# Kernel optimization log

Measured on AMD Instinct MI355X. Metric: run time of the kernel, lower is better.

The kernel has to match this reference:

```python
import jax, jax.numpy as jnp
import numpy as np

D = 1024          # d_model
EXPAND = 2
DI = EXPAND * D   # d_inner = 2048
K = 4             # d_conv
B, L = 4, 2048
EPS = 1e-6


def setup_inputs() -> dict:
    key = jax.random.key(0)
    ks = jax.random.split(key, 16)
    n = lambda i, shape, scale=0.02: (jax.random.normal(ks[i], shape, jnp.float32) * scale)
    return {
        "x": jax.random.normal(ks[0], (B, L, D), jnp.float32),
        "norm_w": jnp.ones((D,), jnp.float32),
        "up_w": n(1, (D, DI)), "up_b": jnp.zeros((DI,), jnp.float32),
        "gate_w": n(2, (D, DI)), "gate_b": jnp.zeros((DI,), jnp.float32),
        "down_w": n(3, (DI, D)), "down_b": jnp.zeros((D,), jnp.float32),
        "conv_w": n(4, (DI, K), 0.2), "conv_b": jnp.zeros((DI,), jnp.float32),
        "wq": n(5, (D, D)), "wk": n(6, (D, D)), "wv": n(7, (D, D)), "wo": n(8, (D, D)),
        "decay": jnp.float32(0.99),
    }


def _rmsnorm(x, w):
    return x * jax.lax.rsqrt(jnp.mean(x * x, axis=-1, keepdims=True) + EPS) * w


def _forward(x, norm_w, up_w, up_b, gate_w, gate_b, down_w, down_b,
             conv_w, conv_b, wq, wk, wv, wo, decay):
    normed = _rmsnorm(x, norm_w)                              # [B,L,D]
    h = normed @ up_w + up_b                                  # [B,L,DI]
    # causal depthwise conv1d: left-pad K-1, groups = DI
    di = conv_w.shape[0]
    kern = conv_w.T[:, None, :]                               # [K,1,DI] (WIO)
    h = jax.lax.conv_general_dilated(
        h, kern, window_strides=(1,), padding=[(conv_w.shape[1] - 1, 0)],
        dimension_numbers=("NWC", "WIO", "NWC"), feature_group_count=di)
    h = jax.nn.silu(h + conv_b)                               # [B,L,DI]
    # gated MLP combine + down-projection
    out = (h * jax.nn.silu(normed @ gate_w + gate_b)) @ down_w + down_b  # [B,L,D]
    # Hebbian associative memory: M_t = decay*M_{t-1} + k_t^T v_t; y_t = q_t M_t
    q = out @ wq; k = out @ wk; v = out @ wv                  # [B,L,D]
    M0 = jnp.zeros((out.shape[0], out.shape[-1], out.shape[-1]), out.dtype)

    def step(M, qkv):
        qt, kt, vt = qkv                                      # each [B,D]
        M = decay * M + jnp.einsum("bd,be->bde", kt, vt)
        return M, jnp.einsum("bd,bde->be", qt, M)

    _, ys = jax.lax.scan(step, M0, (q.swapaxes(0, 1), k.swapaxes(0, 1), v.swapaxes(0, 1)))
    mem_out = ys.swapaxes(0, 1) @ wo                          # [B,L,D]
    return x + mem_out


def reference(x, norm_w, up_w, up_b, gate_w, gate_b, down_w, down_b,
              conv_w, conv_b, wq, wk, wv, wo, decay):
    return _forward(x, norm_w, up_w, up_b, gate_w, gate_b, down_w, down_b,
                    conv_w, conv_b, wq, wk, wv, wo, decay)
```

## Files before the change

### kernel.cpp

```cpp
#include <hip/hip_runtime.h>


typedef __bf16 bf16x8 __attribute__((ext_vector_type(8)));
typedef unsigned short u16x8 __attribute__((ext_vector_type(8)));
typedef float f32x4 __attribute__((ext_vector_type(4)));

constexpr int Bb = 4, Ll = 2048, Dd = 1024, DIc = 2048;
constexpr long LD  = (long)Ll * Dd;
constexpr long BLD = (long)Bb * LD;

static __device__ __forceinline__ unsigned short f2bf(float f) {
  unsigned u = __builtin_bit_cast(unsigned, f);
  u += 0x7fffu + ((u >> 16) & 1u);
  return (unsigned short)(u >> 16);
}
static __device__ __forceinline__ float bf2f(unsigned short u) {
  return __builtin_bit_cast(float, (unsigned)u << 16);
}
static __device__ __forceinline__ float silu(float g) {
  return g / (1.f + __expf(-g));
}

enum { EP_UG = 0, EP_DOWN, EP_GV, EP_DECAY, EP_YO };

#define STAGE_A(DBUF, MG, KH, TILE) {                                          \
    const int kt_ = ((TILE) < NTm1 ? (TILE) : NTm1);                           \
    __builtin_amdgcn_global_load_lds(                                          \
      (const __attribute__((address_space(1))) void*)                          \
        (Ag + (size_t)(aRow + (MG)*64) * lda + kt_*64 + (KH)*32 + aCol),       \
      (__attribute__((address_space(3))) void*)                                \
        (lds + (DBUF)*ADB + (KH)*AKH + (aRb + (MG)*4)*512), 16, 0, 0); }

#define STAGE_B(DBUF, NH, KH, TILE) {                                          \
    const int kt_ = ((TILE) < NTm1 ? (TILE) : NTm1);                           \
    __builtin_amdgcn_global_load_lds(                                          \
      (const __attribute__((address_space(1))) void*)                          \
        (Bg + (size_t)(bRow + (NH)*128) * ldb + kt_*64 + (KH)*32 + aCol),      \
      (__attribute__((address_space(3))) void*)                                \
        (lds + BOFF + (DBUF)*16384 + (KH)*8192 + ((NH)*8 + w)*512), 16, 0, 0); }

#define LOAD_A(DBUF, KS, MG) {                                                 \
  _Pragma("unroll") for (int j_ = 0; j_ < 4; ++j_)                             \
    af[j_] = *(const bf16x8*)&lds[(DBUF)*ADB + (KS)*AKH +                      \
        (aRdBase + (MG)*4 + j_)*512 + fr*32 + cph]; }

#define LOAD_B(DBUF, KS) {                                                     \
  _Pragma("unroll") for (int n_ = 0; n_ < 4; ++n_)                             \
    bfr[KS][n_] = *(const bf16x8*)&lds[BOFF + (DBUF)*16384 + (KS)*8192 +       \
        (bRb + n_)*512 + fr*32 + cph]; }

#define MFMA_PH(KS, MG) {                                                      \
  __builtin_amdgcn_s_setprio(1);                                               \
  _Pragma("unroll") for (int j_ = 0; j_ < 4; ++j_)                             \
  _Pragma("unroll") for (int n_ = 0; n_ < 4; ++n_)                             \
    acc[(MG)*4 + j_][n_] = __builtin_amdgcn_mfma_f32_16x16x32_bf16(            \
        af[j_], bfr[KS][n_], acc[(MG)*4 + j_][n_], 0, 0, 0);                   \
  __builtin_amdgcn_s_setprio(0); }

#define BAR() __builtin_amdgcn_s_barrier()
#define WAIT_LGKM0() { asm volatile("s_waitcnt lgkmcnt(0)" ::: "memory");      \
                       __builtin_amdgcn_sched_barrier(0); }
#define WAIT_LGKM8() asm volatile("s_waitcnt lgkmcnt(8)" ::: "memory")
#define WAIT_VM(N) asm volatile("s_waitcnt vmcnt(" #N ")" ::: "memory")

template <int EPI, int BM>
__global__ __launch_bounds__(512, 2) void gemm8_k(
    const ushort* __restrict__ A, const ushort* __restrict__ Bm,
    void* __restrict__ O0, const float* __restrict__ bias,
    const float* __restrict__ bias2,
    int K, int lda, int ldb, int ldc,
    long sA, long sB, long sC,
    void* __restrict__ O1) {
  constexpr int MF = BM / 32;
  constexpr int ADB = BM * 64;
  constexpr int AKH = BM * 32;
  constexpr int BOFF = BM * 128;
  __shared__ ushort lds[BM == 256 ? 65536 : 49152];

  const int z = blockIdx.z;
  const int gx = gridDim.x;
  const int nwg = gx * gridDim.y;
  const int id = blockIdx.y * gx + blockIdx.x;
  const int chunk = nwg >> 3;
  const int swz = (id & 7) * chunk + (id >> 3);
  const int m0 = (swz / gx) * BM;
  const int n0 = (swz % gx) * 256;

  const int t = threadIdx.x;
  const int lane = t & 63;
  const int w = t >> 6;

  const ushort* Ag = A + (size_t)z * sA + (size_t)m0 * lda;
  const ushort* Bg = Bm + (size_t)z * sB + (size_t)n0 * ldb;

  const int NT = K >> 6;
  const int NTm1 = NT - 1;
  const int NI = NT >> 1;

  const int lp = lane ^ (((lane >> 5) & 1) << 1);
  const int aCol = (lp & 3) * 8;
  const int bRow = (w >> 2) * 64 + (w & 3) * 16 + (lp >> 2);
  int aRow, aRb, aRdBase;
  if constexpr (BM == 256) {
    aRow = (w >> 2) * 128 + (w & 3) * 16 + (lp >> 2);
    aRb = (w >> 2) * 8 + (w & 3);
    aRdBase = (w >> 2) * 8;
  } else {
    aRow = w * 16 + (lp >> 2);
    aRb = w;
    aRdBase = (w >> 2) * 4;
  }
  const int fr = lane & 15;
  const int kg = (lane >> 4) * 8;
  const int cph = kg ^ (((fr >> 3) & 1) << 4);
  const int bRb = ((w & 3) >> 1) * 8 + ((w & 3) & 1) * 4;

  f32x4 acc[MF][4] = {};
  bf16x8 af[4], bfr[2][4];

  if constexpr (BM == 256) {
    STAGE_A(0, 0, 0, 0); STAGE_A(0, 0, 1, 0); STAGE_A(0, 1, 0, 0); STAGE_A(0, 1, 1, 0);
    STAGE_B(0, 0, 0, 0); STAGE_B(0, 0, 1, 0); STAGE_B(0, 1, 0, 0); STAGE_B(0, 1, 1, 0);
    STAGE_B(1, 0, 0, 1); STAGE_B(1, 0, 1, 1); STAGE_B(1, 1, 0, 1); STAGE_B(1, 1, 1, 1);
    STAGE_A(1, 0, 0, 1); STAGE_A(1, 0, 1, 1);
    WAIT_VM(6);
    BAR();
    for (int i = 0; i < NI; ++i) {
      const int tt = 2 * i;
      LOAD_B(0, 0); LOAD_B(0, 1); LOAD_A(0, 0, 0);
      STAGE_A(1, 1, 0, tt + 1); STAGE_A(1, 1, 1, tt + 1);
      WAIT_LGKM8();
      BAR(); WAIT_LGKM0();
      MFMA_PH(0, 0);
      BAR();
      LOAD_A(0, 0, 1);
      STAGE_B(0, 0, 0, tt + 2); STAGE_B(0, 1, 0, tt + 2);
      BAR(); WAIT_LGKM0();
      MFMA_PH(0, 1);
      BAR();
      LOAD_A(0, 1, 0);
      STAGE_B(0, 0, 1, tt + 2); STAGE_B(0, 1, 1, tt + 2);
      BAR(); WAIT_LGKM0();
      MFMA_PH(1, 0);
      BAR();
      LOAD_A(0, 1, 1);
      STAGE_A(0, 0, 0, tt + 2); STAGE_A(0, 0, 1, tt + 2);
      WAIT_VM(6);
      BAR(); WAIT_LGKM0();
      MFMA_PH(1, 1);
      BAR();
      LOAD_B(1, 0); LOAD_B(1, 1); LOAD_A(1, 0, 0);
      STAGE_A(0, 1, 0, tt + 2); STAGE_A(0, 1, 1, tt + 2);
      WAIT_LGKM8();
      BAR(); WAIT_LGKM0();
      MFMA_PH(0, 0);
      BAR();
      LOAD_A(1, 0, 1);
      STAGE_B(1, 0, 0, tt + 3); STAGE_B(1, 1, 0, tt + 3);
      BAR(); WAIT_LGKM0();
      MFMA_PH(0, 1);
      BAR();
      LOAD_A(1, 1, 0);
      STAGE_B(1, 0, 1, tt + 3); STAGE_B(1, 1, 1, tt + 3);
      BAR(); WAIT_LGKM0();
      MFMA_PH(1, 0);
      BAR();
      LOAD_A(1, 1, 1);
      STAGE_A(1, 0, 0, tt + 3); STAGE_A(1, 0, 1, tt + 3);
      WAIT_VM(6);
      BAR(); WAIT_LGKM0();
      MFMA_PH(1, 1);
      BAR();
    }
  } else {
    STAGE_A(0, 0, 0, 0); STAGE_A(0, 0, 1, 0);
    STAGE_B(0, 0, 0, 0); STAGE_B(0, 1, 0, 0); STAGE_B(0, 0, 1, 0); STAGE_B(0, 1, 1, 0);
    STAGE_B(1, 0, 0, 1); STAGE_B(1, 1, 0, 1); STAGE_B(1, 0, 1, 1); STAGE_B(1, 1, 1, 1);
    WAIT_VM(4);
    BAR();
    for (int i = 0; i < NI; ++i) {
      const int tt = 2 * i;
      LOAD_B(0, 0); LOAD_B(0, 1); LOAD_A(0, 0, 0);
      STAGE_A(1, 0, 0, tt + 1); STAGE_A(1, 0, 1, tt + 1);
      WAIT_LGKM8();
      BAR(); WAIT_LGKM0();
      MFMA_PH(0, 0);
      BAR();
      LOAD_A(0, 1, 0);
      STAGE_B(0, 0, 0, tt + 2); STAGE_B(0, 1, 0, tt + 2);
      STAGE_B(0, 0, 1, tt + 2); STAGE_B(0, 1, 1, tt + 2);
      WAIT_VM(4);
      BAR(); WAIT_LGKM0();
      MFMA_PH(1, 0);
      BAR();
      LOAD_B(1, 0); LOAD_B(1, 1); LOAD_A(1, 0, 0);
      STAGE_A(0, 0, 0, tt + 2); STAGE_A(0, 0, 1, tt + 2);
      WAIT_LGKM8();
      BAR(); WAIT_LGKM0();
      MFMA_PH(0, 0);
      BAR();
      LOAD_A(1, 1, 0);
      STAGE_B(1, 0, 0, tt + 3); STAGE_B(1, 1, 0, tt + 3);
      STAGE_B(1, 0, 1, tt + 3); STAGE_B(1, 1, 1, tt + 3);
      WAIT_VM(4);
      BAR(); WAIT_LGKM0();
      MFMA_PH(1, 0);
      BAR();
    }
  }

  const int rb4 = (lane >> 4) * 4;
  const int wm = (w >> 2) * (BM / 2), wn = (w & 3) * 64;

#pragma unroll
  for (int mf = 0; mf < MF; ++mf) {
#pragma unroll
    for (int nf = 0; nf < 4; ++nf) {
      const int gm0 = m0 + wm + mf * 16 + rb4;
      const int gn = n0 + wn + nf * 16 + fr;
      if constexpr (EPI == EP_GV) {
        if (gn < 1024) {
#pragma unroll
          for (int r = 0; r < 4; ++r)
            ((ushort*)O0)[(size_t)(gm0 + r) * 1024 + gn] = f2bf(acc[mf][nf][r]);
        } else {
          const int d = gn - 1024, b = gm0 >> 11, ttp = gm0 & 2047;
          ushort4 w4;
          w4.x = f2bf(acc[mf][nf][0]); w4.y = f2bf(acc[mf][nf][1]);
          w4.z = f2bf(acc[mf][nf][2]); w4.w = f2bf(acc[mf][nf][3]);
          *(ushort4*)&((ushort*)O1)[(size_t)b * LD + (size_t)d * Ll + ttp] = w4;
        }
      } else {
#pragma unroll
        for (int r = 0; r < 4; ++r) {
          const int gm = gm0 + r;
          const size_t idx = (size_t)z * sC + (size_t)gm * ldc + gn;
          const float v = acc[mf][nf][r];
          if constexpr (EPI == EP_UG) {
            const float b = (gn < 2048) ? bias[gn] : bias2[gn - 2048];
            ((ushort*)O0)[idx] = f2bf(v + b);
          } else {
            ((ushort*)O0)[idx] = f2bf(v + bias[gn]);
          }
        }
      }
    }
  }
}

#define S4A(DBUF, MG, KH, TILE) {                                              \
    const int kt_ = ((TILE) < NTm1 ? (TILE) : NTm1);                           \
    __builtin_amdgcn_global_load_lds(                                          \
      (const __attribute__((address_space(1))) void*)                          \
        (Ag + (size_t)(sRow + (MG)*64) * lda + kt_*64 + (KH)*32 + sCol),       \
      (__attribute__((address_space(3))) void*)                                \
        (lds + (DBUF)*8192 + (KH)*4096 + ((MG)*4 + w4)*512), 16, 0, 0); }

#define S4B(DBUF, NH, KH, TILE) {                                              \
    const int kt_ = ((TILE) < NTm1 ? (TILE) : NTm1);                           \
    __builtin_amdgcn_global_load_lds(                                          \
      (const __attribute__((address_space(1))) void*)                          \
        (Bg + (size_t)(sRow + (NH)*64) * ldb + kt_*64 + (KH)*32 + sCol),       \
      (__attribute__((address_space(3))) void*)                                \
        (lds + 16384 + (DBUF)*8192 + (KH)*4096 + ((NH)*4 + w4)*512), 16, 0, 0); }

#define L4A(DBUF, KS) {                                                        \
  _Pragma("unroll") for (int j_ = 0; j_ < 4; ++j_)                             \
    af[j_] = *(const bf16x8*)&lds[(DBUF)*8192 + (KS)*4096 +                    \
        (aRd + j_)*512 + fr*32 + cph]; }

#define L4B(DBUF, KS) {                                                        \
  _Pragma("unroll") for (int n_ = 0; n_ < 4; ++n_)                             \
    bfr[KS][n_] = *(const bf16x8*)&lds[16384 + (DBUF)*8192 + (KS)*4096 +       \
        (bRd + n_)*512 + fr*32 + cph]; }

#define MFMA4(KS) {                                                            \
  __builtin_amdgcn_s_setprio(1);                                               \
  _Pragma("unroll") for (int j_ = 0; j_ < 4; ++j_)                             \
  _Pragma("unroll") for (int n_ = 0; n_ < 4; ++n_)                             \
    acc[j_][n_] = __builtin_amdgcn_mfma_f32_16x16x32_bf16(                     \
        af[j_], bfr[KS][n_], acc[j_][n_], 0, 0, 0);                            \
  __builtin_amdgcn_s_setprio(0); }

template <int EPI>
__global__ __launch_bounds__(256, 2) void gemm4_k(
    const ushort* __restrict__ A, const ushort* __restrict__ Bm,
    void* __restrict__ O0, const float* __restrict__ xres,
    const float* __restrict__ decayp,
    int K, int lda, int ldb, int ldc, long sA, long sB, long sC) {
  __shared__ ushort lds[32768];

  const int t = threadIdx.x;
  const int lane = t & 63;
  const int w4 = t >> 6;

  int z, m0, n0;
  if constexpr (EPI == EP_YO) {
    const int id = blockIdx.y * gridDim.x + blockIdx.x;
    const int half = id >> 8;
    const int u = id & 255;
    const int nt = u & 7;
    const int rem = u >> 3;
    z = rem >> 3;
    const int i8 = rem & 7;
    const int mt = half ? (15 - i8) : i8;
    m0 = mt * 128;
    n0 = nt * 128;
  } else {
    z = blockIdx.z;
    const int gx = gridDim.x;
    const int nwg = gx * gridDim.y;
    const int id = blockIdx.y * gx + blockIdx.x;
    const int chunk = nwg >> 3;
    const int swz = (id & 7) * chunk + (id >> 3);
    m0 = (swz / gx) * 128;
    n0 = (swz % gx) * 128;
    if (n0 > m0) return;
  }

  const ushort* Ag = A + (size_t)z * sA + (size_t)m0 * lda;
  const ushort* Bg = Bm + (size_t)z * sB + (size_t)n0 * ldb;

  int Kend = K;
  if constexpr (EPI == EP_YO) Kend = m0 + 128;
  const int NT = Kend >> 6;
  const int NTm1 = NT - 1;
  const int NI = NT >> 1;

  const int lp = lane ^ (((lane >> 5) & 1) << 1);
  const int sRow = w4 * 16 + (lp >> 2);
  const int sCol = (lp & 3) * 8;
  const int fr = lane & 15;
  const int kg = (lane >> 4) * 8;
  const int cph = kg ^ (((fr >> 3) & 1) << 4);
  const int aRd = (w4 >> 1) * 4;
  const int bRd = (w4 & 1) * 4;

  f32x4 acc[4][4] = {};
  bf16x8 af[4], bfr[2][4];

  S4A(0, 0, 0, 0); S4A(0, 1, 0, 0); S4A(0, 0, 1, 0); S4A(0, 1, 1, 0);
  S4B(0, 0, 0, 0); S4B(0, 1, 0, 0); S4B(0, 0, 1, 0); S4B(0, 1, 1, 0);
  S4B(1, 0, 0, 1); S4B(1, 1, 0, 1); S4B(1, 0, 1, 1); S4B(1, 1, 1, 1);
  WAIT_VM(4);
  BAR();
  for (int i = 0; i < NI; ++i) {
    const int tt = 2 * i;
    L4B(0, 0); L4B(0, 1); L4A(0, 0);
    S4A(1, 0, 0, tt + 1); S4A(1, 1, 0, tt + 1);
    S4A(1, 0, 1, tt + 1); S4A(1, 1, 1, tt + 1);
    WAIT_LGKM8();
    BAR(); WAIT_LGKM0();
    MFMA4(0);
    BAR();
    L4A(0, 1);
    S4B(0, 0, 0, tt + 2); S4B(0, 1, 0, tt + 2);
    S4B(0, 0, 1, tt + 2); S4B(0, 1, 1, tt + 2);
    WAIT_VM(4);
    BAR(); WAIT_LGKM0();
    MFMA4(1);
    BAR();
    L4B(1, 0); L4B(1, 1); L4A(1, 0);
    S4A(0, 0, 0, tt + 2); S4A(0, 1, 0, tt + 2);
    S4A(0, 0, 1, tt + 2); S4A(0, 1, 1, tt + 2);
    WAIT_LGKM8();
    BAR(); WAIT_LGKM0();
    MFMA4(0);
    BAR();
    L4A(1, 1);
    S4B(1, 0, 0, tt + 3); S4B(1, 1, 0, tt + 3);
    S4B(1, 0, 1, tt + 3); S4B(1, 1, 1, tt + 3);
    WAIT_VM(4);
    BAR(); WAIT_LGKM0();
    MFMA4(1);
    BAR();
  }

  const int rb4 = (lane >> 4) * 4;
  const int wm = (w4 >> 1) * 64, wn = (w4 & 1) * 64;
  float logd = 0.f;
  if constexpr (EPI == EP_DECAY) logd = __logf(decayp[0]);

#pragma unroll
  for (int mf = 0; mf < 4; ++mf) {
#pragma unroll
    for (int nf = 0; nf < 4; ++nf) {
      const int gm0 = m0 + wm + mf * 16 + rb4;
      const int gn = n0 + wn + nf * 16 + fr;
#pragma unroll
      for (int r = 0; r < 4; ++r) {
        const int gm = gm0 + r;
        const size_t idx = (size_t)z * sC + (size_t)gm * ldc + gn;
        const float v = acc[mf][nf][r];
        if constexpr (EPI == EP_DECAY) {
          ((ushort*)O0)[idx] =
              (gn <= gm) ? f2bf(v * __expf((float)(gm - gn) * logd)) : (ushort)0;
        } else {
          ((float*)O0)[idx] = v + xres[idx];
        }
      }
    }
  }
}

__global__ __launch_bounds__(256) void prep_k(
    const float* __restrict__ up_w, const float* __restrict__ gate_w,
    const float* __restrict__ down_w, const float* __restrict__ wq,
    const float* __restrict__ wk, const float* __restrict__ wv,
    const float* __restrict__ wo, const float* __restrict__ conv_w,
    const float* __restrict__ x, const float* __restrict__ norm_w,
    ushort* __restrict__ ugw, ushort* __restrict__ down_wT,
    ushort* __restrict__ wq_bf, ushort* __restrict__ wk_bf,
    ushort* __restrict__ wv_bf, ushort* __restrict__ wo_T,
    ushort* __restrict__ cwT, ushort* __restrict__ nrm) {
  const int bid = blockIdx.x;
  const int t = threadIdx.x;
  if (bid < 7168) {
    const float* src; ushort* dst; int R, C, idx;
    if (bid < 2048)      { src = up_w;   dst = ugw;               R = 1024; C = 2048; idx = bid; }
    else if (bid < 4096) { src = gate_w; dst = ugw + 2048 * 1024; R = 1024; C = 2048; idx = bid - 2048; }
    else if (bid < 6144) { src = down_w; dst = down_wT;           R = 2048; C = 1024; idx = bid - 4096; }
    else                 { src = wo;     dst = wo_T;              R = 1024; C = 1024; idx = bid - 6144; }
    __shared__ float tile[32][33];
    const int tx = t & 31, ty = t >> 5;
    const int tilesx = C >> 5;
    const int c0 = (idx % tilesx) * 32, r0 = (idx / tilesx) * 32;
#pragma unroll
    for (int i = 0; i < 4; ++i)
      tile[ty + i * 8][tx] = src[(size_t)(r0 + ty + i * 8) * C + c0 + tx];
    __syncthreads();
#pragma unroll
    for (int i = 0; i < 4; ++i)
      dst[(size_t)(c0 + ty + i * 8) * R + r0 + tx] = f2bf(tile[tx][ty + i * 8]);
  } else if (bid < 10240) {
    const int seg = (bid - 7168) >> 10;
    const int idx = (bid - 7168) & 1023;
    const float* src = (seg == 0) ? wq : (seg == 1) ? wk : wv;
    ushort* dst = (seg == 0) ? wq_bf : (seg == 1) ? wk_bf : wv_bf;
    const size_t e = (size_t)idx * 1024 + t * 4;
    const float4 v = *(const float4*)(src + e);
    ushort4 r;
    r.x = f2bf(v.x); r.y = f2bf(v.y); r.z = f2bf(v.z); r.w = f2bf(v.w);
    *(ushort4*)(dst + e) = r;
  } else if (bid < 10248) {
    const int c = (bid - 10240) * 256 + t;
    const float4 v = *(const float4*)(conv_w + c * 4);
    cwT[0 * DIc + c] = f2bf(v.x);
    cwT[1 * DIc + c] = f2bf(v.y);
    cwT[2 * DIc + c] = f2bf(v.z);
    cwT[3 * DIc + c] = f2bf(v.w);
  } else {
    const int row = bid - 10248;
    const float* xr = x + (size_t)row * Dd;
    const float4 v = *(const float4*)(xr + t * 4);
    float ss = v.x * v.x + v.y * v.y + v.z * v.z + v.w * v.w;
#pragma unroll
    for (int m = 32; m; m >>= 1) ss += __shfl_xor(ss, m);
    __shared__ float red[4];
    if ((t & 63) == 0) red[t >> 6] = ss;
    __syncthreads();
    const float total = red[0] + red[1] + red[2] + red[3];
    const float rs = rsqrtf(total * (1.f / (float)Dd) + 1e-6f);
    const float4 wt = *(const float4*)(norm_w + t * 4);
    ushort4 r;
    r.x = f2bf(v.x * rs * wt.x); r.y = f2bf(v.y * rs * wt.y);
    r.z = f2bf(v.z * rs * wt.z); r.w = f2bf(v.w * rs * wt.w);
    *(ushort4*)(nrm + (size_t)row * Dd + t * 4) = r;
  }
}

__global__ __launch_bounds__(256) void conv_gate_k(
    const ushort* __restrict__ ug, const ushort* __restrict__ cwT,
    const float* __restrict__ cb, ushort* __restrict__ o,
    const ushort* __restrict__ wk_bf, const ushort* __restrict__ wq_bf,
    const ushort* __restrict__ wo_T, const ushort* __restrict__ wv_bf,
    ushort* __restrict__ WsT, ushort* __restrict__ Wv2T) {
  const int bid = blockIdx.x;
  const int t = threadIdx.x;
  if (bid < 128) {
    __shared__ ushort lds[8192];
    ushort* As = lds;
    ushort* Bs = lds + 4096;
    const int oo = bid >> 6, lid = bid & 63;
    const int m0 = (lid >> 3) * 128, n0 = (lid & 7) * 128;
    const ushort* A = (oo ? wo_T : wk_bf) + (size_t)m0 * 1024;
    const ushort* B = (oo ? wv_bf : wq_bf) + (size_t)n0 * 1024;
    ushort* C = oo ? Wv2T : WsT;
    const int lane = t & 63, wave = t >> 6;
    const int wm = (wave >> 1) * 64, wn = (wave & 1) * 64;
    const int fr = lane & 15, kg = (lane >> 4) * 8;
    const int srow0 = wave * 16 + (lane >> 2), scol = (lane & 3) * 8;
    f32x4 acc[4][4] = {};
    for (int k0 = 0; k0 < 1024; k0 += 32) {
#pragma unroll
      for (int p = 0; p < 2; ++p) {
        __builtin_amdgcn_global_load_lds(
            (const __attribute__((address_space(1))) void*)
                (A + (size_t)(srow0 + p * 64) * 1024 + k0 + scol),
            (__attribute__((address_space(3))) void*)(As + (p * 4 + wave) * 512),
            16, 0, 0);
        __builtin_amdgcn_global_load_lds(
            (const __attribute__((address_space(1))) void*)
                (B + (size_t)(srow0 + p * 64) * 1024 + k0 + scol),
            (__attribute__((address_space(3))) void*)(Bs + (p * 4 + wave) * 512),
            16, 0, 0);
      }
      __syncthreads();
      bf16x8 af[4], bv[4];
#pragma unroll
      for (int i = 0; i < 4; ++i) {
        af[i] = *(const bf16x8*)&As[(wm + i * 16 + fr) * 32 + kg];
        bv[i] = *(const bf16x8*)&Bs[(wn + i * 16 + fr) * 32 + kg];
      }
#pragma unroll
      for (int mi = 0; mi < 4; ++mi)
#pragma unroll
        for (int ni = 0; ni < 4; ++ni)
          acc[mi][ni] = __builtin_amdgcn_mfma_f32_16x16x32_bf16(
              af[mi], bv[ni], acc[mi][ni], 0, 0, 0);
      __syncthreads();
    }
    const int rb = (lane >> 4) * 4;
#pragma unroll
    for (int mi = 0; mi < 4; ++mi)
#pragma unroll
      for (int ni = 0; ni < 4; ++ni)
#pragma unroll
        for (int r = 0; r < 4; ++r)
          C[(size_t)(m0 + wm + mi * 16 + rb + r) * 1024 + n0 + wn + ni * 16 + fr] =
              f2bf(acc[mi][ni][r]);
    return;
  }

  const int cbid = bid - 128;
  const int cg = t & 31;
  const int ts = t >> 5;
  const int cblk = cbid & 7;
  const int rblk = cbid >> 3;
  const int c = cblk * 256 + cg * 8;
  const int row0 = rblk * 64 + ts * 8;

  u16x8 w[4];
#pragma unroll
  for (int k = 0; k < 4; ++k) w[k] = *(const u16x8*)&cwT[k * DIc + c];
  float wb[8];
  *(float4*)&wb[0] = *(const float4*)(cb + c);
  *(float4*)&wb[4] = *(const float4*)(cb + c + 4);

  u16x8 h3, h2, h1;
  if ((row0 & (Ll - 1)) == 0) {
    h3 = (u16x8){}; h2 = (u16x8){}; h1 = (u16x8){};
  } else {
    h3 = *(const u16x8*)&ug[(size_t)(row0 - 3) * 4096 + c];
    h2 = *(const u16x8*)&ug[(size_t)(row0 - 2) * 4096 + c];
    h1 = *(const u16x8*)&ug[(size_t)(row0 - 1) * 4096 + c];
  }

#pragma unroll
  for (int i = 0; i < 8; ++i) {
    const size_t rbase = (size_t)(row0 + i) * 4096;
    const u16x8 h0 = *(const u16x8*)&ug[rbase + c];
    const u16x8 g  = *(const u16x8*)&ug[rbase + 2048 + c];
    u16x8 ov;
#pragma unroll
    for (int j = 0; j < 8; ++j) {
      float acc = wb[j];
      acc += bf2f(w[0][j]) * bf2f(h3[j]);
      acc += bf2f(w[1][j]) * bf2f(h2[j]);
      acc += bf2f(w[2][j]) * bf2f(h1[j]);
      acc += bf2f(w[3][j]) * bf2f(h0[j]);
      ov[j] = f2bf(silu(acc) * silu(bf2f(g[j])));
    }
    *(u16x8*)&o[(size_t)(row0 + i) * DIc + c] = ov;
    h3 = h2; h2 = h1; h1 = h0;
  }
}

extern "C" void kernel_launch(void* const* d_in, const int* in_sizes, int n_in,
                              void* d_out, int out_size, void* d_ws,
                              size_t ws_size, hipStream_t stream) {
  const float* x      = (const float*)d_in[0];
  const float* norm_w = (const float*)d_in[1];
  const float* up_w   = (const float*)d_in[2];
  const float* up_b   = (const float*)d_in[3];
  const float* gate_w = (const float*)d_in[4];
  const float* gate_b = (const float*)d_in[5];
  const float* down_w = (const float*)d_in[6];
  const float* down_b = (const float*)d_in[7];
  const float* conv_w = (const float*)d_in[8];
  const float* conv_b = (const float*)d_in[9];
  const float* wq     = (const float*)d_in[10];
  const float* wk     = (const float*)d_in[11];
  const float* wv     = (const float*)d_in[12];
  const float* wo     = (const float*)d_in[13];
  const float* decay  = (const float*)d_in[14];
  float* out = (float*)d_out;
  char* w8 = (char*)d_ws;

  const size_t MiB = 1u << 20;
  ushort* nrm      = (ushort*)(w8 + 0 * MiB);
  ushort* ug       = (ushort*)(w8 + 16 * MiB);
  ushort* S        = (ushort*)(w8 + 16 * MiB);
  ushort* combined = (ushort*)(w8 + 80 * MiB);
  ushort* G        = (ushort*)(w8 + 112 * MiB);
  ushort* vT       = (ushort*)(w8 + 144 * MiB);
  ushort* ugw      = (ushort*)(w8 + 176 * MiB);
  ushort* down_wT  = (ushort*)(w8 + 184 * MiB);
  ushort* wq_bf    = (ushort*)(w8 + 188 * MiB);
  ushort* wk_bf    = (ushort*)(w8 + 190 * MiB);
  ushort* wv_bf    = (ushort*)(w8 + 192 * MiB);
  ushort* wo_T     = (ushort*)(w8 + 194 * MiB);
  ushort* WsT      = (ushort*)(w8 + 196 * MiB);
  ushort* Wv2T     = (ushort*)(w8 + 198 * MiB);
  ushort* cwT      = (ushort*)(w8 + 200 * MiB);

  prep_k<<<18440, 256, 0, stream>>>(up_w, gate_w, down_w, wq, wk, wv, wo,
                                    conv_w, x, norm_w,
                                    ugw, down_wT, wq_bf, wk_bf, wv_bf, wo_T,
                                    cwT, nrm);

  gemm8_k<EP_UG, 256><<<dim3(16, 32), 512, 0, stream>>>(
      nrm, ugw, ug, up_b, gate_b,
      1024, 1024, 1024, 4096, 0, 0, 0, nullptr);

  conv_gate_k<<<1152, 256, 0, stream>>>(ug, cwT, conv_b, combined,
                                        wk_bf, wq_bf, wo_T, wv_bf, WsT, Wv2T);

  gemm8_k<EP_DOWN, 128><<<dim3(4, 64), 512, 0, stream>>>(
      combined, down_wT, nrm, down_b, nullptr,
      2048, 2048, 2048, 1024, 0, 0, 0, nullptr);

  gemm8_k<EP_GV, 256><<<dim3(8, 32), 512, 0, stream>>>(
      nrm, WsT, G, nullptr, nullptr,
      1024, 1024, 1024, 1024, 0, 0, 0, vT);

  gemm4_k<EP_DECAY><<<dim3(16, 16, Bb), 256, 0, stream>>>(
      G, nrm, S, nullptr, decay,
      1024, 1024, 1024, 2048, LD, LD, (long)Ll * Ll);

  gemm4_k<EP_YO><<<dim3(8, 64), 256, 0, stream>>>(
      S, vT, out, x, nullptr,
      0, 2048, 2048, 1024, (long)Ll * Ll, LD, LD);
}
```

Before: 273.7 us.

## Split-K the causal S·V GEMM with atomic float accumulation into prefilled output

The final causal S@V GEMM moves from the 256-thread 128x128 kernel to the 512-thread 128x256 kernel. The K dimension is split into 512-wide chunks so that long lower-triangle rows get more workgroups, which balances the triangular work across a flat 640-block grid. Partial results are combined with float atomicAdd into the output, and the prep kernel now writes x into out up front to supply the residual. This trades atomic traffic and extra output writes for better load balance, and float atomics make the summation order nondeterministic.

After: 321.9 us. 1.18x slower.

```diff
diff --git a/kernel.cpp b/kernel.cpp
--- a/kernel.cpp
+++ b/kernel.cpp
@@ -77,23 +77,43 @@
   constexpr int BOFF = BM * 128;
   __shared__ ushort lds[BM == 256 ? 65536 : 49152];
 
-  const int z = blockIdx.z;
-  const int gx = gridDim.x;
-  const int nwg = gx * gridDim.y;
-  const int id = blockIdx.y * gx + blockIdx.x;
-  const int chunk = nwg >> 3;
-  const int swz = (id & 7) * chunk + (id >> 3);
-  const int m0 = (swz / gx) * BM;
-  const int n0 = (swz % gx) * 256;
-
   const int t = threadIdx.x;
   const int lane = t & 63;
   const int w = t >> 6;
 
-  const ushort* Ag = A + (size_t)z * sA + (size_t)m0 * lda;
-  const ushort* Bg = Bm + (size_t)z * sB + (size_t)n0 * ldb;
-
-  const int NT = K >> 6;
+  int z = blockIdx.z, m0, n0, kd0 = 0, Klen = K;
+  if constexpr (EPI == EP_YO) {
+    const int id = blockIdx.x;
+    z = id / 160;
+    int rem = id - z * 160;
+    const int nt = rem / 40;
+    const int li = rem - nt * 40;
+    int g, off;
+    if (li < 4)       { g = 0; off = li; }
+    else if (li < 12) { g = 1; off = li - 4; }
+    else if (li < 24) { g = 2; off = li - 12; }
+    else              { g = 3; off = li - 24; }
+    const int mt = g * 4 + off / (g + 1);
+    const int kc = off % (g + 1);
+    m0 = mt * 128;
+    n0 = nt * 256;
+    kd0 = kc * 512;
+    Klen = (mt + 1) * 128 - kd0;
+    if (Klen > 512) Klen = 512;
+  } else {
+    const int gx = gridDim.x;
+    const int nwg = gx * gridDim.y;
+    const int id = blockIdx.y * gx + blockIdx.x;
+    const int chunk = nwg >> 3;
+    const int swz = (id & 7) * chunk + (id >> 3);
+    m0 = (swz / gx) * BM;
+    n0 = (swz % gx) * 256;
+  }
+
+  const ushort* Ag = A + (size_t)z * sA + (size_t)m0 * lda + kd0;
+  const ushort* Bg = Bm + (size_t)z * sB + (size_t)n0 * ldb + kd0;
+
+  const int NT = Klen >> 6;
   const int NTm1 = NT - 1;
   const int NI = NT >> 1;
 
@@ -239,8 +259,10 @@
           if constexpr (EPI == EP_UG) {
             const float b = (gn < 2048) ? bias[gn] : bias2[gn - 2048];
             ((ushort*)O0)[idx] = f2bf(v + b);
+          } else if constexpr (EPI == EP_DOWN) {
+            ((ushort*)O0)[idx] = f2bf(v + bias[gn]);
           } else {
-            ((ushort*)O0)[idx] = f2bf(v + bias[gn]);
+            atomicAdd(((float*)O0) + idx, v);
           }
         }
       }
@@ -282,11 +304,9 @@
         af[j_], bfr[KS][n_], acc[j_][n_], 0, 0, 0);                            \
   __builtin_amdgcn_s_setprio(0); }
 
-template <int EPI>
 __global__ __launch_bounds__(256, 2) void gemm4_k(
     const ushort* __restrict__ A, const ushort* __restrict__ Bm,
-    void* __restrict__ O0, const float* __restrict__ xres,
-    const float* __restrict__ decayp,
+    void* __restrict__ O0, const float* __restrict__ decayp,
     int K, int lda, int ldb, int ldc, long sA, long sB, long sC) {
   __shared__ ushort lds[32768];
 
@@ -294,36 +314,20 @@
   const int lane = t & 63;
   const int w4 = t >> 6;
 
-  int z, m0, n0;
-  if constexpr (EPI == EP_YO) {
-    const int id = blockIdx.y * gridDim.x + blockIdx.x;
-    const int half = id >> 8;
-    const int u = id & 255;
-    const int nt = u & 7;
-    const int rem = u >> 3;
-    z = rem >> 3;
-    const int i8 = rem & 7;
-    const int mt = half ? (15 - i8) : i8;
-    m0 = mt * 128;
-    n0 = nt * 128;
-  } else {
-    z = blockIdx.z;
-    const int gx = gridDim.x;
-    const int nwg = gx * gridDim.y;
-    const int id = blockIdx.y * gx + blockIdx.x;
-    const int chunk = nwg >> 3;
-    const int swz = (id & 7) * chunk + (id >> 3);
-    m0 = (swz / gx) * 128;
-    n0 = (swz % gx) * 128;
-    if (n0 > m0) return;
-  }
+  const int z = blockIdx.z;
+  const int gx = gridDim.x;
+  const int nwg = gx * gridDim.y;
+  const int id = blockIdx.y * gx + blockIdx.x;
+  const int chunk = nwg >> 3;
+  const int swz = (id & 7) * chunk + (id >> 3);
+  const int m0 = (swz / gx) * 128;
+  const int n0 = (swz % gx) * 128;
+  if (n0 > m0) return;
 
   const ushort* Ag = A + (size_t)z * sA + (size_t)m0 * lda;
   const ushort* Bg = Bm + (size_t)z * sB + (size_t)n0 * ldb;
 
-  int Kend = K;
-  if constexpr (EPI == EP_YO) Kend = m0 + 128;
-  const int NT = Kend >> 6;
+  const int NT = K >> 6;
   const int NTm1 = NT - 1;
   const int NI = NT >> 1;
 
@@ -378,8 +382,7 @@
 
   const int rb4 = (lane >> 4) * 4;
   const int wm = (w4 >> 1) * 64, wn = (w4 & 1) * 64;
-  float logd = 0.f;
-  if constexpr (EPI == EP_DECAY) logd = __logf(decayp[0]);
+  const float logd = __logf(decayp[0]);
 
 #pragma unroll
   for (int mf = 0; mf < 4; ++mf) {
@@ -391,13 +394,9 @@
       for (int r = 0; r < 4; ++r) {
         const int gm = gm0 + r;
         const size_t idx = (size_t)z * sC + (size_t)gm * ldc + gn;
-        const float v = acc[mf][nf][r];
-        if constexpr (EPI == EP_DECAY) {
-          ((ushort*)O0)[idx] =
-              (gn <= gm) ? f2bf(v * __expf((float)(gm - gn) * logd)) : (ushort)0;
-        } else {
-          ((float*)O0)[idx] = v + xres[idx];
-        }
+        ((ushort*)O0)[idx] =
+            (gn <= gm) ? f2bf(acc[mf][nf][r] * __expf((float)(gm - gn) * logd))
+                       : (ushort)0;
       }
     }
   }
@@ -412,7 +411,8 @@
     ushort* __restrict__ ugw, ushort* __restrict__ down_wT,
     ushort* __restrict__ wq_bf, ushort* __restrict__ wk_bf,
     ushort* __restrict__ wv_bf, ushort* __restrict__ wo_T,
-    ushort* __restrict__ cwT, ushort* __restrict__ nrm) {
+    ushort* __restrict__ cwT, ushort* __restrict__ nrm,
+    float* __restrict__ outp) {
   const int bid = blockIdx.x;
   const int t = threadIdx.x;
   if (bid < 7168) {
@@ -453,6 +453,7 @@
     const int row = bid - 10248;
     const float* xr = x + (size_t)row * Dd;
     const float4 v = *(const float4*)(xr + t * 4);
+    *(float4*)(outp + (size_t)row * Dd + t * 4) = v;
     float ss = v.x * v.x + v.y * v.y + v.z * v.z + v.w * v.w;
 #pragma unroll
     for (int m = 32; m; m >>= 1) ss += __shfl_xor(ss, m);
@@ -617,7 +618,7 @@
   prep_k<<<18440, 256, 0, stream>>>(up_w, gate_w, down_w, wq, wk, wv, wo,
                                     conv_w, x, norm_w,
                                     ugw, down_wT, wq_bf, wk_bf, wv_bf, wo_T,
-                                    cwT, nrm);
+                                    cwT, nrm, out);
 
   gemm8_k<EP_UG, 256><<<dim3(16, 32), 512, 0, stream>>>(
       nrm, ugw, ug, up_b, gate_b,
@@ -634,11 +635,11 @@
       nrm, WsT, G, nullptr, nullptr,
       1024, 1024, 1024, 1024, 0, 0, 0, vT);
 
-  gemm4_k<EP_DECAY><<<dim3(16, 16, Bb), 256, 0, stream>>>(
-      G, nrm, S, nullptr, decay,
+  gemm4_k<<<dim3(16, 16, Bb), 256, 0, stream>>>(
+      G, nrm, S, decay,
       1024, 1024, 1024, 2048, LD, LD, (long)Ll * Ll);
 
-  gemm4_k<EP_YO><<<dim3(8, 64), 256, 0, stream>>>(
-      S, vT, out, x, nullptr,
-      0, 2048, 2048, 1024, (long)Ll * Ll, LD, LD);
-}
+  gemm8_k<EP_YO, 128><<<dim3(640, 1), 512, 0, stream>>>(
+      S, vT, out, nullptr, nullptr,
+      0, 2048, 2048, 1024, (long)Ll * Ll, LD, LD, nullptr);
+}
```
